# Kernel optimization log

Measured on AMD Instinct MI355X. Metric: run time of the kernel, lower is better.

The kernel has to match this reference:

```python
import jax, jax.numpy as jnp
import numpy as np

HID = 2048
N_HEADS = 16
N_KV = 16
HEAD_DIM = HID // N_HEADS
N_EXP = 8
TOP_K = 2
MOE_I = 1408
SH_I = 5632
EPS = 1e-6
ROPE_THETA = 1e6


def _rms(x, w):
    v = jnp.mean(jnp.square(x), axis=-1, keepdims=True)
    return (x * jax.lax.rsqrt(v + EPS)) * w


def _rope(q, k):
    # q, k: [B, S, H, D]
    S, D = q.shape[1], q.shape[-1]
    inv = 1.0 / (ROPE_THETA ** (jnp.arange(0, D, 2, dtype=jnp.float32) / D))
    freqs = jnp.arange(S, dtype=jnp.float32)[:, None] * inv[None, :]   # [S, D/2]
    emb = jnp.concatenate([freqs, freqs], axis=-1)                      # [S, D]
    cos = jnp.cos(emb)[None, :, None, :]
    sin = jnp.sin(emb)[None, :, None, :]
    def rot(t):
        t1, t2 = t[..., : D // 2], t[..., D // 2:]
        return jnp.concatenate([-t2, t1], axis=-1)
    return q * cos + rot(q) * sin, k * cos + rot(k) * sin


def setup_inputs() -> dict:
    key = jax.random.key(0)
    ks = jax.random.split(key, 20)
    s = 0.02
    d = {
        "x": jax.random.normal(ks[0], (2, 1024, HID), jnp.float32),
        "w_ln1": jnp.ones((HID,), jnp.float32),
        "wq": jax.random.normal(ks[1], (HID, N_HEADS * HEAD_DIM), jnp.float32) * s,
        "bq": jnp.zeros((N_HEADS * HEAD_DIM,), jnp.float32),
        "wk": jax.random.normal(ks[2], (HID, N_KV * HEAD_DIM), jnp.float32) * s,
        "bk": jnp.zeros((N_KV * HEAD_DIM,), jnp.float32),
        "wv": jax.random.normal(ks[3], (HID, N_KV * HEAD_DIM), jnp.float32) * s,
        "bv": jnp.zeros((N_KV * HEAD_DIM,), jnp.float32),
        "wo": jax.random.normal(ks[4], (N_HEADS * HEAD_DIM, HID), jnp.float32) * s,
        "w_ln2": jnp.ones((HID,), jnp.float32),
        "w_router": jax.random.normal(ks[5], (HID, N_EXP), jnp.float32) * s,
        "w_gate_e": jax.random.normal(ks[6], (N_EXP, HID, MOE_I), jnp.float32) * s,
        "w_up_e": jax.random.normal(ks[7], (N_EXP, HID, MOE_I), jnp.float32) * s,
        "w_down_e": jax.random.normal(ks[8], (N_EXP, MOE_I, HID), jnp.float32) * s,
        "w_sh_gate": jax.random.normal(ks[9], (HID, SH_I), jnp.float32) * s,
        "w_sh_up": jax.random.normal(ks[10], (HID, SH_I), jnp.float32) * s,
        "w_sh_down": jax.random.normal(ks[11], (SH_I, HID), jnp.float32) * s,
        "w_sh_eg": jax.random.normal(ks[12], (HID, 1), jnp.float32) * s,
    }
    return d


def reference(x, w_ln1, wq, bq, wk, bk, wv, bv, wo, w_ln2, w_router,
              w_gate_e, w_up_e, w_down_e, w_sh_gate, w_sh_up, w_sh_down, w_sh_eg):
    B, S, H = x.shape
    # ---- self-attention (pre-norm) ----
    h = _rms(x, w_ln1)
    q = (h @ wq + bq).reshape(B, S, N_HEADS, HEAD_DIM)
    k = (h @ wk + bk).reshape(B, S, N_KV, HEAD_DIM)
    v = (h @ wv + bv).reshape(B, S, N_KV, HEAD_DIM)
    q, k = _rope(q, k)
    rep = N_HEADS // N_KV
    if rep > 1:
        k = jnp.repeat(k, rep, axis=2)
        v = jnp.repeat(v, rep, axis=2)
    scores = jnp.einsum("bqhd,bkhd->bhqk", q, k) * (HEAD_DIM ** -0.5)
    causal = jnp.tril(jnp.ones((S, S), bool))
    scores = jnp.where(causal[None, None], scores, jnp.finfo(scores.dtype).min)
    attn = jax.nn.softmax(scores, axis=-1)
    ctx = jnp.einsum("bhqk,bkhd->bqhd", attn, v).reshape(B, S, N_HEADS * HEAD_DIM)
    x = x + ctx @ wo

    # ---- sparse MoE FFN (pre-norm) ----
    h = _rms(x, w_ln2).reshape(B * S, H)                     # [T, H]
    logits = h @ w_router                                     # [T, E]
    probs = jax.nn.softmax(logits, axis=-1)
    top_w, top_i = jax.lax.top_k(probs, TOP_K)               # norm_topk_prob=False
    combine = jnp.sum(jax.nn.one_hot(top_i, N_EXP, dtype=h.dtype)
                      * top_w[..., None], axis=1)            # [T, E]
    # dense per-expert compute combined with routing weights (same math as
    # the sorted grouped-GEMM dispatch in Qwen2MoeMLPStack)
    g = jnp.einsum("th,ehi->eti", h, w_gate_e)               # [E, T, I]
    u = jnp.einsum("th,ehi->eti", h, w_up_e)
    y = jnp.einsum("eti,eih->eth", jax.nn.silu(g) * u, w_down_e)
    routed = jnp.einsum("eth,te->th", y, combine)            # [T, H]
    # shared expert with sigmoid gate
    sh = (jax.nn.silu(h @ w_sh_gate) * (h @ w_sh_up)) @ w_sh_down
    sh = sh * jax.nn.sigmoid(h @ w_sh_eg)
    x = x + (routed + sh).reshape(B, S, H)
    return x
```

## Files before the change

### kernel.cpp

```cpp
#include <hip/hip_runtime.h>
#include <hip/hip_bf16.h>
#include <math.h>

#define TOKENS 2048
#define HIDDEN 2048
#define NH 16
#define HD 128
#define SEQ 1024
#define MOE_I 1408
#define SH_I 5632
#define K3 6144
#define MAXROWS 5120

typedef __hip_bfloat16 bf16;
typedef short bf16x8 __attribute__((ext_vector_type(8)));
typedef short bf16x4 __attribute__((ext_vector_type(4)));
typedef float f32x4 __attribute__((ext_vector_type(4)));
typedef float f32x16 __attribute__((ext_vector_type(16)));

__device__ __forceinline__ float b2f(bf16 x) { return __bfloat162float(x); }
__device__ __forceinline__ bf16 f2b(float x) { return __float2bfloat16(x); }
__device__ __forceinline__ void split2(float v, short& hi, short& lo) {
    bf16 h = f2b(v);
    bf16 l = f2b(v - b2f(h));
    hi = __builtin_bit_cast(short, h); lo = __builtin_bit_cast(short, l);
}

__device__ __forceinline__ void load_lds16(const void* g, void* l) {
    __builtin_amdgcn_global_load_lds(
        (const __attribute__((address_space(1))) unsigned int*)g,
        (__attribute__((address_space(3))) unsigned int*)l, 16, 0, 0);
}

__global__ __launch_bounds__(256) void rmsnorm3_k(
    const float* __restrict__ x, const float* __restrict__ w, bf16* __restrict__ out)
{
    const int row = blockIdx.x, tid = threadIdx.x;
    const float4* xr = (const float4*)(x + (size_t)row * HIDDEN);
    float4 v1 = xr[tid], v2 = xr[tid + 256];
    float ss = v1.x*v1.x + v1.y*v1.y + v1.z*v1.z + v1.w*v1.w
             + v2.x*v2.x + v2.y*v2.y + v2.z*v2.z + v2.w*v2.w;
    #pragma unroll
    for (int off = 1; off < 64; off <<= 1) ss += __shfl_xor(ss, off);
    __shared__ float ps[4];
    if ((tid & 63) == 0) ps[tid >> 6] = ss;
    __syncthreads();
    float tot = ps[0] + ps[1] + ps[2] + ps[3];
    float r = rsqrtf(tot * (1.0f / HIDDEN) + 1e-6f);
    bf16* o = out + (size_t)row * 4096;
    float vv[8] = {v1.x, v1.y, v1.z, v1.w, v2.x, v2.y, v2.z, v2.w};
    int idx[8]  = {tid*4, tid*4+1, tid*4+2, tid*4+3,
                   1024+tid*4, 1024+tid*4+1, 1024+tid*4+2, 1024+tid*4+3};
    #pragma unroll
    for (int u = 0; u < 8; u++) {
        short hi, lo; split2(vv[u] * r * w[idx[u]], hi, lo);
        o[idx[u]]        = __builtin_bit_cast(bf16, hi);
        o[2048 + idx[u]] = __builtin_bit_cast(bf16, lo);
    }
}

__global__ __launch_bounds__(256) void transpose64_k(
    const float* __restrict__ W, bf16* __restrict__ Wt, int K, int N,
    long zsrc, long zdst)
{
    __shared__ float t[64][65];
    W  += (size_t)blockIdx.z * zsrc;
    Wt += (size_t)blockIdx.z * zdst;
    const int n0 = blockIdx.x * 64, k0 = blockIdx.y * 64;
    const int tid = threadIdx.x;
    #pragma unroll
    for (int i = 0; i < 4; i++) {
        const int idx = tid + 256*i;
        const int r = idx >> 4, q = idx & 15;
        float4 v = *(const float4*)(W + (size_t)(k0 + r) * N + n0 + q*4);
        t[r][q*4+0] = v.x; t[r][q*4+1] = v.y; t[r][q*4+2] = v.z; t[r][q*4+3] = v.w;
    }
    __syncthreads();
    #pragma unroll
    for (int i = 0; i < 4; i++) {
        const int idx = tid + 256*i;
        const int nl = idx >> 4, kc = idx & 15;
        bf16x4 o4;
        #pragma unroll
        for (int j = 0; j < 4; j++)
            o4[j] = __builtin_bit_cast(short, f2b(t[kc*4+j][nl]));
        *(bf16x4*)(Wt + (size_t)(n0 + nl) * K + k0 + kc*4) = o4;
    }
}

__global__ __launch_bounds__(256) void transpose_qkvo_k(
    const float* __restrict__ wq, const float* __restrict__ wk,
    const float* __restrict__ wv, const float* __restrict__ wo,
    bf16* __restrict__ wtqkv, bf16* __restrict__ wt3o)
{
    const int z = blockIdx.z;
    const float* W = (z == 0) ? wq : (z == 1) ? wk : (z == 2) ? wv : wo;
    bf16* Wt2 = (z < 3) ? wtqkv : wt3o;
    const int nOff = (z < 3) ? z * 2048 : 0;
    __shared__ float t[64][65];
    const int n0 = blockIdx.x * 64, k0 = blockIdx.y * 64;
    const int tid = threadIdx.x;
    #pragma unroll
    for (int i = 0; i < 4; i++) {
        const int idx = tid + 256*i;
        const int r = idx >> 4, q = idx & 15;
        float4 v = *(const float4*)(W + (size_t)(k0 + r) * 2048 + n0 + q*4);
        t[r][q*4+0] = v.x; t[r][q*4+1] = v.y; t[r][q*4+2] = v.z; t[r][q*4+3] = v.w;
    }
    __syncthreads();
    #pragma unroll
    for (int i = 0; i < 4; i++) {
        const int idx = tid + 256*i;
        const int nl = idx >> 4, kc = idx & 15;
        bf16x4 h4, l4;
        #pragma unroll
        for (int j = 0; j < 4; j++) {
            short hi, lo; split2(t[kc*4+j][nl], hi, lo);
            h4[j] = hi; l4[j] = lo;
        }
        bf16* o = Wt2 + (size_t)(nOff + n0 + nl) * 4096 + k0 + kc*4;
        *(bf16x4*)o = h4;
        *(bf16x4*)(o + 2048) = l4;
    }
}

__global__ __launch_bounds__(256) void transpose_moegu_k(
    const float* __restrict__ ge, const float* __restrict__ ue, bf16* __restrict__ wtgu)
{
    const int z = blockIdx.z, e = z & 7, isUp = z >> 3;
    const float* W = (isUp ? ue : ge) + (size_t)e * HIDDEN * MOE_I;
    bf16* Wt = wtgu + (size_t)e * 2816 * HIDDEN;
    __shared__ float t[64][65];
    const int n0 = blockIdx.x * 64, k0 = blockIdx.y * 64;
    const int tid = threadIdx.x;
    #pragma unroll
    for (int i = 0; i < 4; i++) {
        const int idx = tid + 256*i;
        const int r = idx >> 4, q = idx & 15;
        float4 v = *(const float4*)(W + (size_t)(k0 + r) * MOE_I + n0 + q*4);
        t[r][q*4+0] = v.x; t[r][q*4+1] = v.y; t[r][q*4+2] = v.z; t[r][q*4+3] = v.w;
    }
    __syncthreads();
    #pragma unroll
    for (int i = 0; i < 4; i++) {
        const int idx = tid + 256*i;
        const int nl = idx >> 4, kc = idx & 15;
        bf16x4 o4;
        #pragma unroll
        for (int j = 0; j < 4; j++)
            o4[j] = __builtin_bit_cast(short, f2b(t[kc*4+j][nl]));
        *(bf16x4*)(Wt + (size_t)(2*(n0 + nl) + isUp) * 2048 + k0 + kc*4) = o4;
    }
}

__global__ __launch_bounds__(256) void transpose_shgu_k(
    const float* __restrict__ sg, const float* __restrict__ su, bf16* __restrict__ dst)
{
    const int isUp = blockIdx.z;
    const float* W = isUp ? su : sg;
    __shared__ float t[64][65];
    const int n0 = blockIdx.x * 64, k0 = blockIdx.y * 64;
    const int tid = threadIdx.x;
    #pragma unroll
    for (int i = 0; i < 4; i++) {
        const int idx = tid + 256*i;
        const int r = idx >> 4, q = idx & 15;
        float4 v = *(const float4*)(W + (size_t)(k0 + r) * SH_I + n0 + q*4);
        t[r][q*4+0] = v.x; t[r][q*4+1] = v.y; t[r][q*4+2] = v.z; t[r][q*4+3] = v.w;
    }
    __syncthreads();
    #pragma unroll
    for (int i = 0; i < 4; i++) {
        const int idx = tid + 256*i;
        const int nl = idx >> 4, kc = idx & 15;
        bf16x4 o4;
        #pragma unroll
        for (int j = 0; j < 4; j++)
            o4[j] = __builtin_bit_cast(short, f2b(t[kc*4+j][nl]));
        *(bf16x4*)(dst + (size_t)(2*(n0 + nl) + isUp) * 2048 + k0 + kc*4) = o4;
    }
}

__global__ __launch_bounds__(256) void gemm_bt(
    const bf16* __restrict__ A, const bf16* __restrict__ Bt,
    float* __restrict__ Cf, bf16* __restrict__ Cb, const float* __restrict__ bias,
    const float* __restrict__ rowsc,
    int M, int N, int K, int ldA, int ldB, int ldC, long zCstride, int limb3, int epi)
{
    __shared__ __align__(16) bf16 As[128 * 64];
    __shared__ __align__(16) bf16 Bs[128 * 64];
    const int tid = threadIdx.x;
    const int lane = tid & 63, wid = tid >> 6;
    const int l32 = lane & 31, lh2 = lane >> 5;
    const int wr = wid >> 1, wc = wid & 1;
    int lid = blockIdx.y * gridDim.x + blockIdx.x;
    {
        const int nwg = gridDim.x * gridDim.y;
        const int q = nwg >> 3, r = nwg & 7;
        const int xcd = lid & 7, idx = lid >> 3;
        lid = (xcd < r ? xcd * (q + 1) : r * (q + 1) + (xcd - r) * q) + idx;
    }
    const int m0 = (lid % gridDim.x) * 128, n0 = (lid / gridDim.x) * 128;
    const int koff = blockIdx.z * K;

    int srow[4], sslot[4];
    #pragma unroll
    for (int i = 0; i < 4; i++) {
        const int c = tid + 256*i;
        srow[i]  = c >> 3;
        sslot[i] = (((c & 7) ^ (srow[i] & 7)) << 3);
    }

    f32x16 acc[2][2];
    #pragma unroll
    for (int m = 0; m < 2; m++)
        #pragma unroll
        for (int n = 0; n < 2; n++)
            #pragma unroll
            for (int j = 0; j < 16; j++) acc[m][n][j] = 0.f;

    for (int k0 = 0; k0 < K; k0 += 64) {
        const int kcat = koff + k0;
        int ka = kcat, kb = kcat;
        if (limb3) {
            ka = (kcat >= 4096) ? kcat - 4096 : kcat;
            kb = (kcat >= 2048) ? kcat - 2048 : kcat;
        }
        __syncthreads();
        #pragma unroll
        for (int i = 0; i < 4; i++) {
            load_lds16(A  + (size_t)(m0 + srow[i]) * ldA + ka + sslot[i], As + (tid + 256*i) * 8);
            load_lds16(Bt + (size_t)(n0 + srow[i]) * ldB + kb + sslot[i], Bs + (tid + 256*i) * 8);
        }
        __syncthreads();
        bf16x8 a[2][4], b[2][4];
        #pragma unroll
        for (int m = 0; m < 2; m++) {
            const int r = wr*64 + m*32 + l32, rx = r & 7;
            #pragma unroll
            for (int kk = 0; kk < 4; kk++)
                a[m][kk] = *(const bf16x8*)&As[r*64 + ((((kk<<1)|lh2) ^ rx) << 3)];
        }
        #pragma unroll
        for (int n = 0; n < 2; n++) {
            const int r = wc*64 + n*32 + l32, rx = r & 7;
            #pragma unroll
            for (int kk = 0; kk < 4; kk++)
                b[n][kk] = *(const bf16x8*)&Bs[r*64 + ((((kk<<1)|lh2) ^ rx) << 3)];
        }
        #pragma unroll
        for (int kk = 0; kk < 4; kk++)
            #pragma unroll
            for (int m = 0; m < 2; m++)
                #pragma unroll
                for (int n = 0; n < 2; n++)
                    acc[m][n] = __builtin_amdgcn_mfma_f32_32x32x16_bf16(a[m][kk], b[n][kk], acc[m][n], 0, 0, 0);
    }

    float* Cz = Cf + (size_t)blockIdx.z * zCstride;
    #pragma unroll
    for (int m = 0; m < 2; m++) {
        const int base_m = m0 + wr*64 + m*32 + 4*lh2;
        #pragma unroll
        for (int n = 0; n < 2; n++) {
            const int gcol = n0 + wc*64 + n*32 + l32;
            #pragma unroll
            for (int reg = 0; reg < 16; reg++) {
                const int grow = base_m + (reg & 3) + 8*(reg >> 2);
                const float v = acc[m][n][reg];
                if (epi == 6) {
                    const float pv = __shfl_xor(v, 1);
                    if (!(l32 & 1)) {
                        const float g = v, u = pv;
                        const float y = rowsc[grow] * g / (1.0f + __expf(-g)) * u;
                        Cb[(size_t)grow * ldC + (gcol >> 1)] = f2b(y);
                    }
                } else {
                    const size_t o = (size_t)grow * ldC + gcol;
                    if (epi == 0)      Cb[o] = f2b(v);
                    else if (epi == 4) Cz[o] = v;
                    else               Cf[o] = v + bias[gcol];
                }
            }
        }
    }
}

__global__ __launch_bounds__(256) void gemm_gu(
    const bf16* __restrict__ A, const bf16* __restrict__ BtAll,
    const int* __restrict__ offc, const int* __restrict__ perm,
    const float* __restrict__ scale, bf16* __restrict__ AB)
{
    const int e = blockIdx.z;
    const int off = offc[8 + e];
    const int padCnt = offc[9 + e] - off;
    const int m0 = blockIdx.x * 128;
    if (m0 >= padCnt) return;
    __shared__ __align__(16) bf16 As[128 * 64];
    __shared__ __align__(16) bf16 Bs[128 * 64];
    const int tid = threadIdx.x;
    const int lane = tid & 63, wid = tid >> 6;
    const int l32 = lane & 31, lh2 = lane >> 5;
    const int wr = wid >> 1, wc = wid & 1;
    const int n0 = blockIdx.y * 128;
    const bf16* Bt = BtAll + (size_t)e * 2816 * 2048;

    int srow[4], sslot[4], tok[4];
    #pragma unroll
    for (int i = 0; i < 4; i++) {
        const int c = tid + 256*i;
        srow[i]  = c >> 3;
        sslot[i] = (((c & 7) ^ (srow[i] & 7)) << 3);
        int t = perm[off + m0 + srow[i]];
        tok[i] = (t < 0) ? 0 : t;
    }

    f32x16 acc[2][2];
    #pragma unroll
    for (int m = 0; m < 2; m++)
        #pragma unroll
        for (int n = 0; n < 2; n++)
            #pragma unroll
            for (int j = 0; j < 16; j++) acc[m][n][j] = 0.f;

    for (int k0 = 0; k0 < 2048; k0 += 64) {
        __syncthreads();
        #pragma unroll
        for (int i = 0; i < 4; i++) {
            load_lds16(A  + (size_t)tok[i] * 2048 + k0 + sslot[i], As + (tid + 256*i) * 8);
            load_lds16(Bt + (size_t)(n0 + srow[i]) * 2048 + k0 + sslot[i], Bs + (tid + 256*i) * 8);
        }
        __syncthreads();
        bf16x8 a[2][4], b[2][4];
        #pragma unroll
        for (int m = 0; m < 2; m++) {
            const int r = wr*64 + m*32 + l32, rx = r & 7;
            #pragma unroll
            for (int kk = 0; kk < 4; kk++)
                a[m][kk] = *(const bf16x8*)&As[r*64 + ((((kk<<1)|lh2) ^ rx) << 3)];
        }
        #pragma unroll
        for (int n = 0; n < 2; n++) {
            const int r = wc*64 + n*32 + l32, rx = r & 7;
            #pragma unroll
            for (int kk = 0; kk < 4; kk++)
                b[n][kk] = *(const bf16x8*)&Bs[r*64 + ((((kk<<1)|lh2) ^ rx) << 3)];
        }
        #pragma unroll
        for (int kk = 0; kk < 4; kk++)
            #pragma unroll
            for (int m = 0; m < 2; m++)
                #pragma unroll
                for (int n = 0; n < 2; n++)
                    acc[m][n] = __builtin_amdgcn_mfma_f32_32x32x16_bf16(a[m][kk], b[n][kk], acc[m][n], 0, 0, 0);
    }

    #pragma unroll
    for (int m = 0; m < 2; m++) {
        const int base_m = m0 + wr*64 + m*32 + 4*lh2;
        #pragma unroll
        for (int n = 0; n < 2; n++) {
            const int gcol = n0 + wc*64 + n*32 + l32;
            #pragma unroll
            for (int reg = 0; reg < 16; reg++) {
                const int grow = base_m + (reg & 3) + 8*(reg >> 2);
                const float v = acc[m][n][reg];
                const float pv = __shfl_xor(v, 1);
                if (!(l32 & 1)) {
                    const float g = v, u = pv;
                    const float y = scale[off + grow] * g / (1.0f + __expf(-g)) * u;
                    AB[(size_t)(off + grow) * MOE_I + (gcol >> 1)] = f2b(y);
                }
            }
        }
    }
}

__global__ __launch_bounds__(256) void gemm_down(
    const bf16* __restrict__ A, const bf16* __restrict__ BtAll,
    const int* __restrict__ offc, bf16* __restrict__ Y)
{
    const int e = blockIdx.z;
    const int off = offc[8 + e];
    const int padCnt = offc[9 + e] - off;
    const int m0 = blockIdx.x * 128;
    if (m0 >= padCnt) return;
    __shared__ __align__(16) bf16 As[128 * 64];
    __shared__ __align__(16) bf16 Bs[128 * 64];
    const int tid = threadIdx.x;
    const int lane = tid & 63, wid = tid >> 6;
    const int l32 = lane & 31, lh2 = lane >> 5;
    const int wr = wid >> 1, wc = wid & 1;
    const int n0 = blockIdx.y * 128;
    const bf16* Bt = BtAll + (size_t)e * 2048 * 1408;

    int srow[4], sslot[4];
    #pragma unroll
    for (int i = 0; i < 4; i++) {
        const int c = tid + 256*i;
        srow[i]  = c >> 3;
        sslot[i] = (((c & 7) ^ (srow[i] & 7)) << 3);
    }

    f32x16 acc[2][2];
    #pragma unroll
    for (int m = 0; m < 2; m++)
        #pragma unroll
        for (int n = 0; n < 2; n++)
            #pragma unroll
            for (int j = 0; j < 16; j++) acc[m][n][j] = 0.f;

    for (int k0 = 0; k0 < 1408; k0 += 64) {
        __syncthreads();
        #pragma unroll
        for (int i = 0; i < 4; i++) {
            load_lds16(A  + (size_t)(off + m0 + srow[i]) * 1408 + k0 + sslot[i], As + (tid + 256*i) * 8);
            load_lds16(Bt + (size_t)(n0 + srow[i]) * 1408 + k0 + sslot[i], Bs + (tid + 256*i) * 8);
        }
        __syncthreads();
        bf16x8 a[2][4], b[2][4];
        #pragma unroll
        for (int m = 0; m < 2; m++) {
            const int r = wr*64 + m*32 + l32, rx = r & 7;
            #pragma unroll
            for (int kk = 0; kk < 4; kk++)
                a[m][kk] = *(const bf16x8*)&As[r*64 + ((((kk<<1)|lh2) ^ rx) << 3)];
        }
        #pragma unroll
        for (int n = 0; n < 2; n++) {
            const int r = wc*64 + n*32 + l32, rx = r & 7;
            #pragma unroll
            for (int kk = 0; kk < 4; kk++)
                b[n][kk] = *(const bf16x8*)&Bs[r*64 + ((((kk<<1)|lh2) ^ rx) << 3)];
        }
        #pragma unroll
        for (int kk = 0; kk < 4; kk++)
            #pragma unroll
            for (int m = 0; m < 2; m++)
                #pragma unroll
                for (int n = 0; n < 2; n++)
                    acc[m][n] = __builtin_amdgcn_mfma_f32_32x32x16_bf16(a[m][kk], b[n][kk], acc[m][n], 0, 0, 0);
    }

    #pragma unroll
    for (int m = 0; m < 2; m++) {
        const int base_m = m0 + wr*64 + m*32 + 4*lh2;
        #pragma unroll
        for (int n = 0; n < 2; n++) {
            const int gcol = n0 + wc*64 + n*32 + l32;
            #pragma unroll
            for (int reg = 0; reg < 16; reg++) {
                const int grow = base_m + (reg & 3) + 8*(reg >> 2);
                Y[(size_t)(off + grow) * 2048 + gcol] = f2b(acc[m][n][reg]);
            }
        }
    }
}

__global__ void rope_table_k(float2* __restrict__ cs)
{
    const int i = blockIdx.x * 256 + threadIdx.x;
    const int s = i >> 6, d = i & 63;
    const float fr = (float)s * powf(1.0e6f, -(float)d * (1.0f / 64.0f));
    float c, sn;
    sincosf(fr, &sn, &c);
    cs[i] = make_float2(c, sn);
}

__global__ __launch_bounds__(256) void transpose_v3_k(
    const float* __restrict__ qkv, bf16* __restrict__ vth, bf16* __restrict__ vtl)
{
    __shared__ float t[32][33];
    const int s0 = blockIdx.x * 32, d0 = blockIdx.y * 32;
    const int bh = blockIdx.z, b = bh >> 4, h = bh & 15;
    const int tx = threadIdx.x & 31, ty = threadIdx.x >> 5;
    const float* vb = qkv + ((size_t)b * SEQ) * 6144 + 4096 + h * HD;
    #pragma unroll
    for (int i = 0; i < 4; i++)
        t[ty + i*8][tx] = vb[(size_t)(s0 + ty + i*8) * 6144 + d0 + tx];
    __syncthreads();
    const size_t ob = ((size_t)bh * HD) * SEQ;
    #pragma unroll
    for (int i = 0; i < 4; i++) {
        float val = t[tx][ty + i*8];
        short hi, lo; split2(val, hi, lo);
        const size_t o = ob + (size_t)(d0 + ty + i*8) * SEQ + s0 + tx;
        vth[o] = __builtin_bit_cast(bf16, hi);
        vtl[o] = __builtin_bit_cast(bf16, lo);
    }
}

__global__ __launch_bounds__(256) void attn3_k(
    const float* __restrict__ qkv, const float2* __restrict__ ropecs,
    const bf16* __restrict__ vthg, const bf16* __restrict__ vtlg,
    bf16* __restrict__ ctx2)
{
    __shared__ __align__(16) bf16 SM[32768];
    bf16* Ksh = SM;
    bf16* Ksl = SM + 8192;
    bf16* Vth = SM + 16384;
    bf16* Vtl = SM + 24576;
    bf16* Ph  = SM;
    bf16* Pl  = SM + 4096;

    const int tid = threadIdx.x, lane = tid & 63, wid = tid >> 6;
    const int l16 = lane & 15, lh = lane >> 4;
    const int bh = blockIdx.y, b = bh >> 4, h = bh & 15;
    const int qbase = blockIdx.x * 64;
    const int qw = qbase + wid * 16;
    const float* qp = qkv + ((size_t)b * SEQ) * 6144 + h * HD;
    const float* kp = qkv + ((size_t)b * SEQ) * 6144 + 2048 + h * HD;
    const bf16* vph = vthg + ((size_t)bh * HD) * SEQ;
    const bf16* vpl = vtlg + ((size_t)bh * HD) * SEQ;

    bf16x8 aqh[4], aql[4];
    {
        float qr[4][8];
        const int tok = qw + l16;
        #pragma unroll
        for (int c = 0; c < 4; c++) {
            const float* qrow = qp + (size_t)tok * 6144 + c*32 + lh*8;
            #pragma unroll
            for (int u = 0; u < 8; u++) qr[c][u] = qrow[u];
        }
        #pragma unroll
        for (int c = 0; c < 2; c++)
            #pragma unroll
            for (int u = 0; u < 8; u++) {
                const int d = c*32 + lh*8 + u;
                const float2 cs_ = ropecs[(tok << 6) | d];
                const float a = qr[c][u], bb = qr[c+2][u];
                qr[c][u]   = a * cs_.x - bb * cs_.y;
                qr[c+2][u] = bb * cs_.x + a * cs_.y;
            }
        #pragma unroll
        for (int c = 0; c < 4; c++)
            #pragma unroll
            for (int u = 0; u < 8; u++) {
                short hi, lo; split2(qr[c][u], hi, lo);
                aqh[c][u] = hi; aql[c][u] = lo;
            }
    }

    f32x4 o[8];
    #pragma unroll
    for (int n = 0; n < 8; n++) o[n] = (f32x4){0.f, 0.f, 0.f, 0.f};
    float mj[4], lj[4];
    #pragma unroll
    for (int j = 0; j < 4; j++) { mj[j] = -1e30f; lj[j] = 0.f; }

    const int kr = tid >> 2;
    const int q16 = tid & 3;
    const int krx = kr & 15;
    const int kt_end = blockIdx.x + 1;
    for (int kt = 0; kt < kt_end; ++kt) {
        const int kv0 = kt * 64;
        __syncthreads();
        {
            const int tokk = kv0 + kr;
            const float* krow = kp + (size_t)tokk * 6144;
            float4 A4[4], B4[4];
            #pragma unroll
            for (int u = 0; u < 4; u++) {
                A4[u] = *(const float4*)(krow + q16*16 + u*4);
                B4[u] = *(const float4*)(krow + 64 + q16*16 + u*4);
            }
            #pragma unroll
            for (int u = 0; u < 4; u++) {
                #pragma unroll
                for (int j = 0; j < 4; j++) {
                    const int d = q16*16 + u*4 + j;
                    const float2 cs_ = ropecs[(tokk << 6) | d];
                    float* pa = ((float*)&A4[u]) + j;
                    float* pb = ((float*)&B4[u]) + j;
                    const float a = *pa, bb = *pb;
                    *pa = a * cs_.x - bb * cs_.y;
                    *pb = bb * cs_.x + a * cs_.y;
                }
                bf16x4 h4, l4, h4b, l4b;
                #pragma unroll
                for (int j = 0; j < 4; j++) {
                    short hi, lo;
                    split2(((float*)&A4[u])[j], hi, lo); h4[j] = hi; l4[j] = lo;
                    split2(((float*)&B4[u])[j], hi, lo); h4b[j] = hi; l4b[j] = lo;
                }
                const int colA = q16*16 + u*4;
                const int sA = ((colA >> 3) ^ krx);
                const int dstA = kr*128 + (sA << 3) + ((u & 1) * 4);
                *(bf16x4*)&Ksh[dstA] = h4;
                *(bf16x4*)&Ksl[dstA] = l4;
                const int colB = 64 + colA;
                const int sB = ((colB >> 3) ^ krx);
                const int dstB = kr*128 + (sB << 3) + ((u & 1) * 4);
                *(bf16x4*)&Ksh[dstB] = h4b;
                *(bf16x4*)&Ksl[dstB] = l4b;
            }
        }
        #pragma unroll
        for (int i = 0; i < 4; i++) {
            const int c = tid + 256*i;
            const int row = c >> 3, sl = (c & 7) ^ (row & 7);
            load_lds16(vph + (size_t)row * SEQ + kv0 + (sl << 3), Vth + c*8);
            load_lds16(vpl + (size_t)row * SEQ + kv0 + (sl << 3), Vtl + c*8);
        }
        __syncthreads();

        f32x4 sg[4];
        #pragma unroll
        for (int g = 0; g < 4; g++) sg[g] = (f32x4){0.f,0.f,0.f,0.f};
        __builtin_amdgcn_s_setprio(1);
        #pragma unroll
        for (int c = 0; c < 4; c++) {
            #pragma unroll
            for (int g = 0; g < 4; g++) {
                const int row = l16 + g*16;
                const int sl = (((c*4 + lh) ^ (row & 15)) << 3);
                bf16x8 bkh = *(const bf16x8*)&Ksh[row*128 + sl];
                bf16x8 bkl = *(const bf16x8*)&Ksl[row*128 + sl];
                sg[g] = __builtin_amdgcn_mfma_f32_16x16x32_bf16(aqh[c], bkh, sg[g], 0, 0, 0);
                sg[g] = __builtin_amdgcn_mfma_f32_16x16x32_bf16(aql[c], bkh, sg[g], 0, 0, 0);
                sg[g] = __builtin_amdgcn_mfma_f32_16x16x32_bf16(aqh[c], bkl, sg[g], 0, 0, 0);
            }
        }
        __builtin_amdgcn_s_setprio(0);
        __syncthreads();

        const float scale = 0.08838834764831845f;
        #pragma unroll
        for (int j = 0; j < 4; j++) {
            const int qrow = qw + lh*4 + j;
            float sv[4];
            #pragma unroll
            for (int g = 0; g < 4; g++) {
                sv[g] = sg[g][j] * scale;
                if (kv0 + l16 + g*16 > qrow) sv[g] = -1e30f;
            }
            float mx = fmaxf(fmaxf(sv[0], sv[1]), fmaxf(sv[2], sv[3]));
            #pragma unroll
            for (int off = 1; off < 16; off <<= 1) mx = fmaxf(mx, __shfl_xor(mx, off, 16));
            const float nm = fmaxf(mj[j], mx);
            const float al = __expf(mj[j] - nm);
            float pg[4], rs = 0.f;
            #pragma unroll
            for (int g = 0; g < 4; g++) { pg[g] = __expf(sv[g] - nm); rs += pg[g]; }
            #pragma unroll
            for (int off = 1; off < 16; off <<= 1) rs += __shfl_xor(rs, off, 16);
            lj[j] = lj[j] * al + rs;
            mj[j] = nm;
            #pragma unroll
            for (int n = 0; n < 8; n++) o[n][j] *= al;
            const int prow = lh*4 + j;
            #pragma unroll
            for (int g = 0; g < 4; g++) {
                short hi, lo; split2(pg[g], hi, lo);
                const int col = l16 + g*16;
                const int addr = wid*1024 + prow*64 + ((((col >> 3) ^ (prow & 7)) << 3)) + (col & 7);
                Ph[addr] = __builtin_bit_cast(bf16, hi);
                Pl[addr] = __builtin_bit_cast(bf16, lo);
            }
        }
        __builtin_amdgcn_s_setprio(1);
        #pragma unroll
        for (int ks = 0; ks < 2; ks++) {
            const int psl = (((ks*4 + lh) ^ (l16 & 7)) << 3);
            bf16x8 aph = *(const bf16x8*)&Ph[wid*1024 + l16*64 + psl];
            bf16x8 apl = *(const bf16x8*)&Pl[wid*1024 + l16*64 + psl];
            #pragma unroll
            for (int n = 0; n < 8; n++) {
                const int row = n*16 + l16;
                const int vsl = (((ks*4 + lh) ^ (row & 7)) << 3);
                bf16x8 bvh = *(const bf16x8*)&Vth[row*64 + vsl];
                bf16x8 bvl = *(const bf16x8*)&Vtl[row*64 + vsl];
                o[n] = __builtin_amdgcn_mfma_f32_16x16x32_bf16(aph, bvh, o[n], 0, 0, 0);
                o[n] = __builtin_amdgcn_mfma_f32_16x16x32_bf16(apl, bvh, o[n], 0, 0, 0);
                o[n] = __builtin_amdgcn_mfma_f32_16x16x32_bf16(aph, bvl, o[n], 0, 0, 0);
            }
        }
        __builtin_amdgcn_s_setprio(0);
    }

    float inv[4];
    #pragma unroll
    for (int j = 0; j < 4; j++) inv[j] = 1.0f / lj[j];
    #pragma unroll
    for (int n = 0; n < 8; n++)
        #pragma unroll
        for (int j = 0; j < 4; j++) {
            const float v = o[n][j] * inv[j];
            short hi, lo; split2(v, hi, lo);
            const size_t base = ((size_t)b * SEQ + (qw + lh*4 + j)) * 4096 + h * HD + n*16 + l16;
            ctx2[base]        = __builtin_bit_cast(bf16, hi);
            ctx2[base + 2048] = __builtin_bit_cast(bf16, lo);
        }
}

__global__ __launch_bounds__(256) void combine_rms_router_k(
    const float* __restrict__ x, const float* __restrict__ xp,
    const float* __restrict__ wln, const float* __restrict__ wr,
    const float* __restrict__ weg,
    float* __restrict__ x1, bf16* __restrict__ h2,
    float* __restrict__ comb, float* __restrict__ sigeg)
{
    const int row = blockIdx.x, tid = threadIdx.x;
    const size_t rb = (size_t)row * HIDDEN;
    const long zs = (long)TOKENS * HIDDEN;
    __shared__ float ps[4];
    __shared__ float pacc[4][9];
    float4 v[2];
    #pragma unroll
    for (int u = 0; u < 2; u++) {
        const int i = tid + u * 256;
        float4 a  = ((const float4*)(x + rb))[i];
        float4 p0 = ((const float4*)(xp + rb))[i];
        float4 p1 = ((const float4*)(xp + zs + rb))[i];
        float4 p2 = ((const float4*)(xp + 2*zs + rb))[i];
        v[u].x = a.x + p0.x + p1.x + p2.x;
        v[u].y = a.y + p0.y + p1.y + p2.y;
        v[u].z = a.z + p0.z + p1.z + p2.z;
        v[u].w = a.w + p0.w + p1.w + p2.w;
        ((float4*)(x1 + rb))[i] = v[u];
    }
    float ss = v[0].x*v[0].x + v[0].y*v[0].y + v[0].z*v[0].z + v[0].w*v[0].w
             + v[1].x*v[1].x + v[1].y*v[1].y + v[1].z*v[1].z + v[1].w*v[1].w;
    #pragma unroll
    for (int off = 1; off < 64; off <<= 1) ss += __shfl_xor(ss, off);
    if ((tid & 63) == 0) ps[tid >> 6] = ss;
    __syncthreads();
    const float tot = ps[0] + ps[1] + ps[2] + ps[3];
    const float r = rsqrtf(tot * (1.0f / HIDDEN) + 1e-6f);

    float acc[9];
    #pragma unroll
    for (int e = 0; e < 9; e++) acc[e] = 0.f;
    #pragma unroll
    for (int u = 0; u < 2; u++) {
        const int i = (tid + u * 256) * 4;
        const float vv[4] = {v[u].x, v[u].y, v[u].z, v[u].w};
        #pragma unroll
        for (int q = 0; q < 4; q++) {
            const float hv = vv[q] * r * wln[i + q];
            h2[rb + i + q] = f2b(hv);
            const float* wrow = wr + (size_t)(i + q) * 8;
            #pragma unroll
            for (int e = 0; e < 8; e++) acc[e] += hv * wrow[e];
            acc[8] += hv * weg[i + q];
        }
    }
    #pragma unroll
    for (int e = 0; e < 9; e++)
        #pragma unroll
        for (int off = 1; off < 64; off <<= 1) acc[e] += __shfl_xor(acc[e], off);
    if ((tid & 63) == 0)
        #pragma unroll
        for (int e = 0; e < 9; e++) pacc[tid >> 6][e] = acc[e];
    __syncthreads();
    if (tid == 0) {
        float lg[9];
        #pragma unroll
        for (int e = 0; e < 9; e++) lg[e] = pacc[0][e] + pacc[1][e] + pacc[2][e] + pacc[3][e];
        float mx = lg[0];
        #pragma unroll
        for (int e = 1; e < 8; e++) mx = fmaxf(mx, lg[e]);
        float p[8], s = 0.f;
        #pragma unroll
        for (int e = 0; e < 8; e++) { p[e] = expf(lg[e] - mx); s += p[e]; }
        const float invs = 1.0f / s;
        #pragma unroll
        for (int e = 0; e < 8; e++) p[e] *= invs;
        int i1 = 0;
        #pragma unroll
        for (int e = 1; e < 8; e++) if (p[e] > p[i1]) i1 = e;
        int i2 = (i1 == 0) ? 1 : 0;
        #pragma unroll
        for (int e = 0; e < 8; e++) if (e != i1 && p[e] > p[i2]) i2 = e;
        #pragma unroll
        for (int e = 0; e < 8; e++)
            comb[(size_t)row * 8 + e] = (e == i1 || e == i2) ? p[e] : 0.f;
        sigeg[row] = 1.0f / (1.0f + expf(-lg[8]));
    }
}

__global__ __launch_bounds__(256) void count_fill_k(
    const float* __restrict__ comb, int* __restrict__ offc, int* __restrict__ perm,
    float* __restrict__ scale, int* __restrict__ inv)
{
    __shared__ int cnt[8], off[9], fil[8];
    const int tid = threadIdx.x;
    if (tid < 8) { cnt[tid] = 0; fil[tid] = 0; }
    __syncthreads();
    for (int t = tid; t < TOKENS; t += 256)
        #pragma unroll
        for (int e = 0; e < 8; e++)
            if (comb[(size_t)t * 8 + e] > 0.f) atomicAdd(&cnt[e], 1);
    __syncthreads();
    if (tid == 0) {
        off[0] = 0;
        for (int e = 0; e < 8; e++) off[e+1] = off[e] + ((cnt[e] + 127) & ~127);
    }
    __syncthreads();
    for (int i = tid; i < MAXROWS; i += 256) { perm[i] = -1; scale[i] = 0.f; }
    __syncthreads();
    for (int t = tid; t < TOKENS; t += 256) {
        int j = 0;
        #pragma unroll
        for (int e = 0; e < 8; e++) {
            const float c = comb[(size_t)t * 8 + e];
            if (c > 0.f) {
                int s = atomicAdd(&fil[e], 1);
                int slot = off[e] + s;
                perm[slot] = t;
                scale[slot] = c;
                inv[t * 2 + j] = slot;
                j++;
            }
        }
    }
    __syncthreads();
    if (tid < 9) offc[8 + tid] = off[tid];
}

__global__ void final_k(const float* __restrict__ x1, const bf16* __restrict__ y,
                        const int* __restrict__ inv, const float* __restrict__ ysh,
                        float* __restrict__ out)
{
    const int i = blockIdx.x * 256 + threadIdx.x;
    const int t = i >> 9;
    const int col = (i & 511) * 4;
    const int s0 = inv[t*2], s1 = inv[t*2 + 1];
    const long zs = (long)TOKENS * HIDDEN;
    float4 a  = ((const float4*)x1)[i];
    float4 h0 = ((const float4*)ysh)[i];
    float4 h1 = ((const float4*)(ysh + zs))[i];
    const bf16* y0 = y + (size_t)s0 * 2048 + col;
    const bf16* y1 = y + (size_t)s1 * 2048 + col;
    float4 r;
    r.x = a.x + h0.x + h1.x + b2f(y0[0]) + b2f(y1[0]);
    r.y = a.y + h0.y + h1.y + b2f(y0[1]) + b2f(y1[1]);
    r.z = a.z + h0.z + h1.z + b2f(y0[2]) + b2f(y1[2]);
    r.w = a.w + h0.w + h1.w + b2f(y0[3]) + b2f(y1[3]);
    ((float4*)out)[i] = r;
}

extern "C" void kernel_launch(void* const* d_in, const int* in_sizes, int n_in,
                              void* d_out, int out_size, void* d_ws, size_t ws_size,
                              hipStream_t stream)
{
    const float* x     = (const float*)d_in[0];
    const float* w_ln1 = (const float*)d_in[1];
    const float* wq    = (const float*)d_in[2];
    const float* bq    = (const float*)d_in[3];
    const float* wk    = (const float*)d_in[4];
    const float* bk    = (const float*)d_in[5];
    const float* wv    = (const float*)d_in[6];
    const float* bv    = (const float*)d_in[7];
    const float* wo    = (const float*)d_in[8];
    const float* w_ln2 = (const float*)d_in[9];
    const float* w_rt  = (const float*)d_in[10];
    const float* w_ge  = (const float*)d_in[11];
    const float* w_ue  = (const float*)d_in[12];
    const float* w_de  = (const float*)d_in[13];
    const float* w_sg  = (const float*)d_in[14];
    const float* w_su  = (const float*)d_in[15];
    const float* w_sd  = (const float*)d_in[16];
    const float* w_eg  = (const float*)d_in[17];
    float* out = (float*)d_out;
    (void)in_sizes; (void)n_in; (void)out_size; (void)ws_size;

    char* ws = (char*)d_ws;
    float* x1    = (float*)(ws + 0);
    bf16*  h2    = (bf16*)(ws + 16777216);
    float* comb  = (float*)(ws + 25165824);
    float* seg   = (float*)(ws + 25231360);
    int*   offc  = (int*)(ws + 25239552);
    float* scale = (float*)(ws + 25243648);
    int*   perm  = (int*)(ws + 25276416);
    int*   inv   = (int*)(ws + 25297920);
    float* bqkv  = (float*)(ws + 25314304);
    float2* ropecs = (float2*)(ws + 25338880);
    const size_t S = 25863168;
    bf16*  hcat  = (bf16*)(ws + S);
    bf16*  wtqkv = (bf16*)(ws + S + 16777216);
    float* qkvf  = (float*)(ws + S + 67108864);
    bf16*  wt3o  = (bf16*)(ws + S + 117440512);
    bf16*  vth   = (bf16*)(ws + S);
    bf16*  vtl   = (bf16*)(ws + S + 8388608);
    bf16*  ctx2  = (bf16*)(ws + S + 16777216);
    float* xp    = (float*)(ws + S + 50331648);
    bf16*  wtgu  = (bf16*)(ws + S);
    bf16*  ab    = (bf16*)(ws + S + 92274688);
    bf16*  wtd   = (bf16*)(ws + S);
    bf16*  ymoe  = (bf16*)(ws + S + 46137344);
    bf16*  wtshgu = (bf16*)(ws + S);
    bf16*  ash    = (bf16*)(ws + S + 67108864);
    bf16*  wtshd  = (bf16*)(ws + S);
    float* ysh    = (float*)(ws + S + 90177536);

    rmsnorm3_k<<<TOKENS, 256, 0, stream>>>(x, w_ln1, hcat);
    (void)hipMemcpyAsync(bqkv,        bq, 8192, hipMemcpyDeviceToDevice, stream);
    (void)hipMemcpyAsync(bqkv + 2048, bk, 8192, hipMemcpyDeviceToDevice, stream);
    (void)hipMemcpyAsync(bqkv + 4096, bv, 8192, hipMemcpyDeviceToDevice, stream);
    rope_table_k<<<256, 256, 0, stream>>>(ropecs);

    transpose_qkvo_k<<<dim3(32, 32, 4), 256, 0, stream>>>(wq, wk, wv, wo, wtqkv, wt3o);
    gemm_bt<<<dim3(16, 48, 1), 256, 0, stream>>>(hcat, wtqkv, qkvf, nullptr, bqkv, nullptr,
                                                 TOKENS, 6144, K3, 4096, 4096, 6144, 0, 1, 5);

    transpose_v3_k<<<dim3(32, 4, 32), 256, 0, stream>>>(qkvf, vth, vtl);
    attn3_k<<<dim3(16, 32), 256, 0, stream>>>(qkvf, ropecs, vth, vtl, ctx2);

    gemm_bt<<<dim3(16, 16, 3), 256, 0, stream>>>(ctx2, wt3o, xp, nullptr, nullptr, nullptr,
                                                 TOKENS, HIDDEN, 2048, 4096, 4096, 2048,
                                                 (long)TOKENS * HIDDEN, 1, 4);
    combine_rms_router_k<<<TOKENS, 256, 0, stream>>>(x, xp, w_ln2, w_rt, w_eg,
                                                     x1, h2, comb, seg);
    count_fill_k<<<1, 256, 0, stream>>>(comb, offc, perm, scale, inv);

    transpose_moegu_k<<<dim3(22, 32, 16), 256, 0, stream>>>(w_ge, w_ue, wtgu);
    gemm_gu<<<dim3(MAXROWS/128, 22, 8), 256, 0, stream>>>(h2, wtgu, offc, perm, scale, ab);
    transpose64_k<<<dim3(32, 22, 8), 256, 0, stream>>>(w_de, wtd, MOE_I, HIDDEN,
                                                       (long)MOE_I*HIDDEN, (long)HIDDEN*MOE_I);
    gemm_down<<<dim3(MAXROWS/128, 16, 8), 256, 0, stream>>>(ab, wtd, offc, ymoe);

    transpose_shgu_k<<<dim3(88, 32, 2), 256, 0, stream>>>(w_sg, w_su, wtshgu);
    gemm_bt<<<dim3(16, 88, 1), 256, 0, stream>>>(h2, wtshgu, nullptr, ash, nullptr, seg,
                                                 TOKENS, 2*SH_I, HIDDEN, HIDDEN, HIDDEN, SH_I, 0, 0, 6);
    transpose64_k<<<dim3(32, 88, 1), 256, 0, stream>>>(w_sd, wtshd, SH_I, HIDDEN, 0, 0);
    gemm_bt<<<dim3(16, 16, 2), 256, 0, stream>>>(ash, wtshd, ysh, nullptr, nullptr, nullptr,
                                                 TOKENS, HIDDEN, SH_I/2, SH_I, SH_I, 2048,
                                                 (long)TOKENS * HIDDEN, 0, 4);

    final_k<<<(TOKENS * HIDDEN) / 1024, 256, 0, stream>>>(x1, ymoe, inv, ysh, out);
}
```

Baseline: 980.0 us.

## Add 256x256-tile 8-wave GEMM with quadrant-phased pipeline for QKV and shared gate/up

```diff
diff --git a/kernel.cpp b/kernel.cpp
--- a/kernel.cpp
+++ b/kernel.cpp
@@ -179,6 +179,146 @@
             o4[j] = __builtin_bit_cast(short, f2b(t[kc*4+j][nl]));
         *(bf16x4*)(dst + (size_t)(2*(n0 + nl) + isUp) * 2048 + k0 + kc*4) = o4;
     }
+}
+
+__global__ __launch_bounds__(512) void gemm256(
+    const bf16* __restrict__ A, const bf16* __restrict__ Bt,
+    float* __restrict__ Cf, bf16* __restrict__ Cb,
+    const float* __restrict__ bias, const float* __restrict__ rowsc,
+    int M, int N, int K, int ldA, int ldB, int ldC, int limb3, int epi)
+{
+    extern __shared__ __align__(16) bf16 LDS[];
+    const int tid = threadIdx.x;
+    const int lane = tid & 63, wid = tid >> 6;
+    const int l32 = lane & 31, lh2 = lane >> 5;
+    const int wm2 = wid >> 2, wn4 = wid & 3;
+    int lid = blockIdx.y * gridDim.x + blockIdx.x;
+    {
+        const int nwg = gridDim.x * gridDim.y;
+        const int q = nwg >> 3, r = nwg & 7;
+        const int xcd = lid & 7, idx = lid >> 3;
+        lid = (xcd < r ? xcd * (q + 1) : r * (q + 1) + (xcd - r) * q) + idx;
+    }
+    const int m0 = (lid % gridDim.x) * 256, n0 = (lid / gridDim.x) * 256;
+    const int NT = K / 64;
+
+    int srow[2], sslot[2];
+    #pragma unroll
+    for (int i = 0; i < 2; i++) {
+        const int c2 = tid + 512*i;
+        srow[i]  = c2 >> 3;
+        sslot[i] = ((c2 & 7) ^ (srow[i] & 7)) << 3;
+    }
+
+#define KMAP(kt, ka_, kb_) \
+    int ka_ = (kt) * 64, kb_ = (kt) * 64; \
+    if (limb3) { if (ka_ >= 4096) ka_ -= 4096; if (kb_ >= 2048) kb_ -= 2048; }
+
+#define STAGE_HALF(op, h, kt, buf) do { \
+    KMAP(kt, ka_, kb_); \
+    const bf16* bas_ = (op) ? Bt : A; \
+    const int gr0_ = ((op) ? n0 : m0) + (h)*128; \
+    const int ld_ = (op) ? ldB : ldA; \
+    const int ks_ = (op) ? kb_ : ka_; \
+    bf16* dst_ = LDS + ((size_t)((buf)*4 + (op)*2 + (h))) * 8192; \
+    _Pragma("unroll") \
+    for (int i_ = 0; i_ < 2; i_++) \
+        load_lds16(bas_ + (size_t)(gr0_ + srow[i_]) * ld_ + ks_ + sslot[i_], \
+                   dst_ + (tid + 512*i_) * 8); \
+} while (0)
+
+    f32x16 acc00[2], acc01[2], acc10[2], acc11[2];
+    #pragma unroll
+    for (int m = 0; m < 2; m++)
+        #pragma unroll
+        for (int j = 0; j < 16; j++) {
+            acc00[m][j] = 0.f; acc01[m][j] = 0.f;
+            acc10[m][j] = 0.f; acc11[m][j] = 0.f;
+        }
+
+    STAGE_HALF(0, 0, 0, 0);
+    STAGE_HALF(1, 0, 0, 0);
+    STAGE_HALF(1, 1, 0, 0);
+    STAGE_HALF(0, 1, 0, 0);
+    if (NT > 1) { STAGE_HALF(0, 0, 1, 1); STAGE_HALF(1, 0, 1, 1); }
+    asm volatile("s_waitcnt vmcnt(4)" ::: "memory");
+    __builtin_amdgcn_s_barrier();
+    asm volatile("" ::: "memory");
+
+#define PHASE(QA, QB, ACC, STAGES) do { \
+    const bf16* As_ = LDS + ((size_t)(c*4 + (QA))) * 8192; \
+    const bf16* Bs_ = LDS + ((size_t)(c*4 + 2 + (QB))) * 8192; \
+    const int rb_ = wn4*32 + l32; \
+    bf16x8 a_[2][4], b_[4]; \
+    _Pragma("unroll") \
+    for (int kk = 0; kk < 4; kk++) { \
+        _Pragma("unroll") \
+        for (int m = 0; m < 2; m++) { \
+            const int r_ = wm2*64 + m*32 + l32; \
+            a_[m][kk] = *(const bf16x8*)&As_[r_*64 + ((((kk<<1)|lh2) ^ (r_&7)) << 3)]; \
+        } \
+        b_[kk] = *(const bf16x8*)&Bs_[rb_*64 + ((((kk<<1)|lh2) ^ (rb_&7)) << 3)]; \
+    } \
+    STAGES; \
+    __builtin_amdgcn_s_barrier(); \
+    asm volatile("" ::: "memory"); \
+    __builtin_amdgcn_s_setprio(1); \
+    _Pragma("unroll") \
+    for (int kk = 0; kk < 4; kk++) { \
+        ACC[0] = __builtin_amdgcn_mfma_f32_32x32x16_bf16(a_[0][kk], b_[kk], ACC[0], 0, 0, 0); \
+        ACC[1] = __builtin_amdgcn_mfma_f32_32x32x16_bf16(a_[1][kk], b_[kk], ACC[1], 0, 0, 0); \
+    } \
+    __builtin_amdgcn_s_setprio(0); \
+    __builtin_amdgcn_s_barrier(); \
+    asm volatile("" ::: "memory"); \
+} while (0)
+
+    for (int kt = 0; kt < NT; kt++) {
+        const int c = kt & 1;
+        PHASE(0, 0, acc00, {
+            if (kt + 1 < NT) { STAGE_HALF(1, 1, kt+1, c^1); STAGE_HALF(0, 1, kt+1, c^1); }
+        });
+        PHASE(0, 1, acc01, {});
+        PHASE(1, 0, acc10, { if (kt + 2 < NT) STAGE_HALF(0, 0, kt+2, c); });
+        PHASE(1, 1, acc11, { if (kt + 2 < NT) STAGE_HALF(1, 0, kt+2, c); });
+        asm volatile("s_waitcnt vmcnt(4)" ::: "memory");
+        __builtin_amdgcn_s_barrier();
+        asm volatile("" ::: "memory");
+    }
+
+#define EPI(QA, QB, ACC) do { \
+    _Pragma("unroll") \
+    for (int m = 0; m < 2; m++) { \
+        const int base_m = m0 + (QA)*128 + wm2*64 + m*32 + 4*lh2; \
+        const int gcol = n0 + (QB)*128 + wn4*32 + l32; \
+        _Pragma("unroll") \
+        for (int reg = 0; reg < 16; reg++) { \
+            const int grow = base_m + (reg & 3) + 8*(reg >> 2); \
+            const float v = ACC[m][reg]; \
+            if (epi == 6) { \
+                const float pv = __shfl_xor(v, 1); \
+                if (!(l32 & 1)) { \
+                    const float g = v, u = pv; \
+                    const float y = rowsc[grow] * g / (1.0f + __expf(-g)) * u; \
+                    Cb[(size_t)grow * ldC + (gcol >> 1)] = f2b(y); \
+                } \
+            } else if (epi == 5) { \
+                Cf[(size_t)grow * ldC + gcol] = v + bias[gcol]; \
+            } else { \
+                Cb[(size_t)grow * ldC + gcol] = f2b(v); \
+            } \
+        } \
+    } \
+} while (0)
+
+    EPI(0, 0, acc00);
+    EPI(0, 1, acc01);
+    EPI(1, 0, acc10);
+    EPI(1, 1, acc11);
+#undef EPI
+#undef PHASE
+#undef STAGE_HALF
+#undef KMAP
 }
 
 __global__ __launch_bounds__(256) void gemm_bt(
@@ -267,20 +407,11 @@
             #pragma unroll
             for (int reg = 0; reg < 16; reg++) {
                 const int grow = base_m + (reg & 3) + 8*(reg >> 2);
+                const size_t o = (size_t)grow * ldC + gcol;
                 const float v = acc[m][n][reg];
-                if (epi == 6) {
-                    const float pv = __shfl_xor(v, 1);
-                    if (!(l32 & 1)) {
-                        const float g = v, u = pv;
-                        const float y = rowsc[grow] * g / (1.0f + __expf(-g)) * u;
-                        Cb[(size_t)grow * ldC + (gcol >> 1)] = f2b(y);
-                    }
-                } else {
-                    const size_t o = (size_t)grow * ldC + gcol;
-                    if (epi == 0)      Cb[o] = f2b(v);
-                    else if (epi == 4) Cz[o] = v;
-                    else               Cf[o] = v + bias[gcol];
-                }
+                if (epi == 0)      Cb[o] = f2b(v);
+                else if (epi == 4) Cz[o] = v;
+                else               Cf[o] = v + bias[gcol];
             }
         }
     }
@@ -902,8 +1033,8 @@
     rope_table_k<<<256, 256, 0, stream>>>(ropecs);
 
     transpose_qkvo_k<<<dim3(32, 32, 4), 256, 0, stream>>>(wq, wk, wv, wo, wtqkv, wt3o);
-    gemm_bt<<<dim3(16, 48, 1), 256, 0, stream>>>(hcat, wtqkv, qkvf, nullptr, bqkv, nullptr,
-                                                 TOKENS, 6144, K3, 4096, 4096, 6144, 0, 1, 5);
+    gemm256<<<dim3(8, 24), 512, 131072, stream>>>(hcat, wtqkv, qkvf, nullptr, bqkv, nullptr,
+                                                  TOKENS, 6144, K3, 4096, 4096, 6144, 1, 5);
 
     transpose_v3_k<<<dim3(32, 4, 32), 256, 0, stream>>>(qkvf, vth, vtl);
     attn3_k<<<dim3(16, 32), 256, 0, stream>>>(qkvf, ropecs, vth, vtl, ctx2);
@@ -922,8 +1053,8 @@
     gemm_down<<<dim3(MAXROWS/128, 16, 8), 256, 0, stream>>>(ab, wtd, offc, ymoe);
 
     transpose_shgu_k<<<dim3(88, 32, 2), 256, 0, stream>>>(w_sg, w_su, wtshgu);
-    gemm_bt<<<dim3(16, 88, 1), 256, 0, stream>>>(h2, wtshgu, nullptr, ash, nullptr, seg,
-                                                 TOKENS, 2*SH_I, HIDDEN, HIDDEN, HIDDEN, SH_I, 0, 0, 6);
+    gemm256<<<dim3(8, 44), 512, 131072, stream>>>(h2, wtshgu, nullptr, ash, nullptr, seg,
+                                                  TOKENS, 2*SH_I, HIDDEN, HIDDEN, HIDDEN, SH_I, 0, 6);
     transpose64_k<<<dim3(32, 88, 1), 256, 0, stream>>>(w_sd, wtshd, SH_I, HIDDEN, 0, 0);
     gemm_bt<<<dim3(16, 16, 2), 256, 0, stream>>>(ash, wtshd, ysh, nullptr, nullptr, nullptr,
                                                  TOKENS, HIDDEN, SH_I/2, SH_I, SH_I, 2048,
```

Result: slower. 1.101 ms (+12.4%).
